# Kernel tuning notes

Measured on AMD Instinct MI355X. Metric: run time of the kernel, lower is better.

The kernel has to match this reference:

```python
import jax, jax.numpy as jnp
import numpy as np

HEADS = 12

def setup_inputs() -> dict:
    key = jax.random.key(0)
    ks = jax.random.split(key, 6)
    dim = 768
    x  = jax.random.normal(ks[0], (2, 4096, dim), dtype=jnp.float32)
    s = dim ** -0.5
    wq = jax.random.normal(ks[1], (dim, dim), dtype=jnp.float32) * s
    wk = jax.random.normal(ks[2], (dim, dim), dtype=jnp.float32) * s
    wv = jax.random.normal(ks[3], (dim, dim), dtype=jnp.float32) * s
    wo = jax.random.normal(ks[4], (dim, dim), dtype=jnp.float32) * s
    bo = jnp.zeros((dim,), dtype=jnp.float32)
    return {"x": x, "wq": wq, "wk": wk, "wv": wv, "wo": wo, "bo": bo}

def reference(x, wq, wk, wv, wo, bo):
    b, n, dim = x.shape
    h = HEADS
    d = dim // h
    scale = d ** -0.5
    # nn.Linear(dim, dim, bias=False): y = x @ W.T ; weights stored [out, in]
    def proj(w):
        return (x @ w.T).reshape(b, n, h, d).transpose(0, 2, 1, 3)  # b h n d
    q, k, v = proj(wq), proj(wk), proj(wv)
    dots = jnp.einsum('bhqd,bhkd->bhqk', q, k) * scale  # full N x N scores
    attn = jax.nn.softmax(dots, axis=-1)
    out = jnp.einsum('bhqk,bhkd->bhqd', attn, v)
    out = out.transpose(0, 2, 1, 3).reshape(b, n, dim)
    # to_out: Linear(dim, dim) + Dropout (identity at inference)
    return out @ wo.T + bo
```

## Files before the change

### kernel.cpp

```cpp
#include <hip/hip_runtime.h>
#include <hip/hip_bf16.h>


#define HEADS 12
#define NSEQ  4096
#define DIM   768
#define DH    64
#define BATCH 2
#define QSCALE 0.18033688f

typedef __attribute__((ext_vector_type(8))) short bf16x8;
typedef __attribute__((ext_vector_type(4))) float f32x4;
typedef __attribute__((ext_vector_type(4))) short bf16x4;

static __device__ __forceinline__ short f2bf(float f) {
    __hip_bfloat16 h = __float2bfloat16(f);
    return *reinterpret_cast<short*>(&h);
}

#define NX (BATCH*NSEQ*DIM)
#define NW (DIM*DIM)

__global__ __launch_bounds__(256) void convert_kernel(
    const float* __restrict__ x,  const float* __restrict__ wq,
    const float* __restrict__ wk, const float* __restrict__ wv,
    const float* __restrict__ wo,
    short* __restrict__ xb, short* __restrict__ wqb, short* __restrict__ wkb,
    short* __restrict__ wvb, short* __restrict__ wob)
{
    int i = (blockIdx.x * 256 + threadIdx.x) * 4;
    const float* src; short* dst; int off;
    if      (i < NX)          { src = x;  dst = xb;  off = i; }
    else if (i < NX + NW)     { src = wq; dst = wqb; off = i - NX; }
    else if (i < NX + 2*NW)   { src = wk; dst = wkb; off = i - NX - NW; }
    else if (i < NX + 3*NW)   { src = wv; dst = wvb; off = i - NX - 2*NW; }
    else                      { src = wo; dst = wob; off = i - NX - 3*NW; }
    float4 f = *(const float4*)(src + off);
    bf16x4 o; o[0] = f2bf(f.x); o[1] = f2bf(f.y); o[2] = f2bf(f.z); o[3] = f2bf(f.w);
    *(bf16x4*)(dst + off) = o;
}

__global__ __launch_bounds__(256, 4) void qkv_proj_kernel(
    const short* __restrict__ xb, const short* __restrict__ wqb,
    const short* __restrict__ wkb, const short* __restrict__ wvb,
    short* __restrict__ qb, short* __restrict__ kb, short* __restrict__ vtb)
{
    __shared__ __align__(16) short As[2][128*32];
    __shared__ __align__(16) short Bs[2][128*32];

    const int wave = threadIdx.x >> 6, lane = threadIdx.x & 63;
    const int lr = lane & 15, lq = lane >> 4;
    const int which = blockIdx.y / 6;
    const short* __restrict__ W = (which == 0) ? wqb : ((which == 1) ? wkb : wvb);
    const int m0  = blockIdx.x * 128;
    const int o0l = (blockIdx.y % 6) * 128;

    const int t  = threadIdx.x;
    const int sr = t >> 2, sc = t & 3;
    const int scs = (sc ^ (sr & 3)) * 8;
    const short* __restrict__ gA = xb + (size_t)(m0  + sr) * DIM + sc*8;
    const short* __restrict__ gB = W  + (size_t)(o0l + sr) * DIM + sc*8;

    const int wm = (wave & 1) * 64, wn = (wave >> 1) * 64;
    const int rsw = (lq ^ (lr & 3)) * 8;

    f32x4 acc[4][4];
    #pragma unroll
    for (int i = 0; i < 4; i++)
        #pragma unroll
        for (int j = 0; j < 4; j++) acc[i][j] = (f32x4){0.f, 0.f, 0.f, 0.f};

    bf16x8 ra0 = *(const bf16x8*)(gA);
    bf16x8 ra1 = *(const bf16x8*)(gA + (size_t)64*DIM);
    bf16x8 rb0 = *(const bf16x8*)(gB);
    bf16x8 rb1 = *(const bf16x8*)(gB + (size_t)64*DIM);
    *(bf16x8*)&As[0][ sr     *32 + scs] = ra0;
    *(bf16x8*)&As[0][(sr+64) *32 + scs] = ra1;
    *(bf16x8*)&Bs[0][ sr     *32 + scs] = rb0;
    *(bf16x8*)&Bs[0][(sr+64) *32 + scs] = rb1;
    __syncthreads();

    for (int kt = 0; kt < 24; kt++) {
        const int p = kt & 1;
        if (kt < 23) {
            const int k1 = (kt + 1) * 32;
            ra0 = *(const bf16x8*)(gA + k1);
            ra1 = *(const bf16x8*)(gA + (size_t)64*DIM + k1);
            rb0 = *(const bf16x8*)(gB + k1);
            rb1 = *(const bf16x8*)(gB + (size_t)64*DIM + k1);
        }
        bf16x8 a[4], b[4];
        #pragma unroll
        for (int i = 0; i < 4; i++)
            a[i] = *(const bf16x8*)&As[p][(wm + i*16 + lr)*32 + rsw];
        #pragma unroll
        for (int j = 0; j < 4; j++)
            b[j] = *(const bf16x8*)&Bs[p][(wn + j*16 + lr)*32 + rsw];
        #pragma unroll
        for (int i = 0; i < 4; i++)
            #pragma unroll
            for (int j = 0; j < 4; j++)
                acc[i][j] = __builtin_amdgcn_mfma_f32_16x16x32_bf16(a[i], b[j], acc[i][j], 0, 0, 0);
        if (kt < 23) {
            *(bf16x8*)&As[1-p][ sr     *32 + scs] = ra0;
            *(bf16x8*)&As[1-p][(sr+64) *32 + scs] = ra1;
            *(bf16x8*)&Bs[1-p][ sr     *32 + scs] = rb0;
            *(bf16x8*)&Bs[1-p][(sr+64) *32 + scs] = rb1;
        }
        __syncthreads();
    }

    if (which == 2) {
        #pragma unroll
        for (int i = 0; i < 4; i++)
            #pragma unroll
            for (int j = 0; j < 4; j++) {
                const int mb = m0 + wm + i*16 + lq*4;
                const int o  = o0l + wn + j*16 + lr;
                const int bb = mb >> 12, n0 = mb & (NSEQ - 1);
                const int h  = o >> 6,   dd = o & 63;
                bf16x4 v;
                #pragma unroll
                for (int r = 0; r < 4; r++) v[r] = f2bf(acc[i][j][r]);
                *(bf16x4*)(vtb + ((size_t)(bb*HEADS + h) * DH + dd) * NSEQ + n0) = v;
            }
    } else {
        short* __restrict__ dst = (which == 0) ? qb : kb;
        const float scale = (which == 0) ? QSCALE : 1.0f;
        #pragma unroll
        for (int i = 0; i < 4; i++)
            #pragma unroll
            for (int j = 0; j < 4; j++)
                #pragma unroll
                for (int r = 0; r < 4; r++) {
                    const int m  = m0 + wm + i*16 + lq*4 + r;
                    const int o  = o0l + wn + j*16 + lr;
                    const int bb = m >> 12, n = m & (NSEQ - 1);
                    const int h  = o >> 6,  dd = o & 63;
                    dst[(((size_t)(bb*HEADS + h) * NSEQ) + n) * DH + dd] = f2bf(acc[i][j][r] * scale);
                }
    }
}

__global__ __launch_bounds__(256, 3) void attn_kernel(
    const short* __restrict__ qb, const short* __restrict__ kb,
    const short* __restrict__ vtb, short* __restrict__ ob)
{
    __shared__ __align__(16) short Ks[2][64*64];
    __shared__ __align__(16) short Vs[2][64*64];
    __shared__ __align__(16) short Vones[16*64];
    __shared__ __align__(16) short Ps[4][2][16*64];

    const int wave = threadIdx.x >> 6, lane = threadIdx.x & 63;
    const int lrow = lane & 15, lquad = lane >> 4;

    const int flat = blockIdx.x;
    const int xcd  = flat & 7;
    const int idx  = flat >> 3;
    const int bh   = xcd * 3 + (idx % 3);
    const int qblk = idx / 3;
    const int b = bh / HEADS, h = bh % HEADS;
    const int q0 = qblk * 128 + wave * 32;

    const short* __restrict__ Q  = qb  + (size_t)bh * NSEQ * DH;
    const short* __restrict__ K  = kb  + (size_t)bh * NSEQ * DH;
    const short* __restrict__ Vt = vtb + (size_t)bh * DH * NSEQ;

    for (int i = threadIdx.x; i < 16*64; i += 256) Vones[i] = 0x3F80;

    const int t  = threadIdx.x;
    const int r2 = t >> 3, cc = t & 7;
    const int ccs = (cc ^ (r2 & 7)) * 8;

    bf16x8 aq[2][2];
    #pragma unroll
    for (int rb = 0; rb < 2; rb++)
        #pragma unroll
        for (int kk = 0; kk < 2; kk++)
            aq[rb][kk] = *(const bf16x8*)(Q + (size_t)(q0 + rb*16 + lrow) * DH + kk*32 + lquad*8);

    f32x4 oacc[2][5];
    #pragma unroll
    for (int rb = 0; rb < 2; rb++)
        #pragma unroll
        for (int ct = 0; ct < 5; ct++) oacc[rb][ct] = (f32x4){0.f, 0.f, 0.f, 0.f};

    {
        bf16x8 k0a = *(const bf16x8*)(K  + (size_t)(r2     ) * DH   + cc*8);
        bf16x8 k0b = *(const bf16x8*)(K  + (size_t)(r2 + 32) * DH   + cc*8);
        bf16x8 v0a = *(const bf16x8*)(Vt + (size_t)(r2     ) * NSEQ + cc*8);
        bf16x8 v0b = *(const bf16x8*)(Vt + (size_t)(r2 + 32) * NSEQ + cc*8);
        *(bf16x8*)&Ks[0][ r2     *64 + ccs] = k0a;
        *(bf16x8*)&Ks[0][(r2+32) *64 + ccs] = k0b;
        *(bf16x8*)&Vs[0][ r2     *64 + ccs] = v0a;
        *(bf16x8*)&Vs[0][(r2+32) *64 + ccs] = v0b;
    }
    __syncthreads();

    for (int kt = 0; kt < NSEQ / 64; kt++) {
        const int p = kt & 1;
        bf16x8 kr0, kr1, vr0, vr1;
        if (kt + 1 < NSEQ / 64) {
            const int key1 = (kt + 1) * 64;
            kr0 = *(const bf16x8*)(K  + (size_t)(key1 + r2     ) * DH   + cc*8);
            kr1 = *(const bf16x8*)(K  + (size_t)(key1 + r2 + 32) * DH   + cc*8);
            vr0 = *(const bf16x8*)(Vt + (size_t)(r2     ) * NSEQ + key1 + cc*8);
            vr1 = *(const bf16x8*)(Vt + (size_t)(r2 + 32) * NSEQ + key1 + cc*8);
        }

        bf16x8 ak[4][2];
        #pragma unroll
        for (int ct = 0; ct < 4; ct++)
            #pragma unroll
            for (int kk = 0; kk < 2; kk++)
                ak[ct][kk] = *(const bf16x8*)&Ks[p][(ct*16 + lrow)*64 + (((kk*4 + lquad) ^ (lrow & 7)) * 8)];

        #pragma unroll
        for (int rb = 0; rb < 2; rb++) {
            f32x4 s[4];
            #pragma unroll
            for (int ct = 0; ct < 4; ct++) s[ct] = (f32x4){0.f, 0.f, 0.f, 0.f};
            #pragma unroll
            for (int kk = 0; kk < 2; kk++)
                #pragma unroll
                for (int ct = 0; ct < 4; ct++)
                    s[ct] = __builtin_amdgcn_mfma_f32_16x16x32_bf16(ak[ct][kk], aq[rb][kk], s[ct], 0, 0, 0);
            #pragma unroll
            for (int ct = 0; ct < 4; ct++) {
                bf16x4 pk;
                #pragma unroll
                for (int r = 0; r < 4; r++) pk[r] = f2bf(exp2f(s[ct][r]));
                const int cps = (((ct*2 + (lquad >> 1)) ^ (lrow & 7)) * 8) + (lquad & 1) * 4;
                *(bf16x4*)&Ps[wave][rb][lrow*64 + cps] = pk;
            }
        }

        bf16x8 bv[5][2];
        #pragma unroll
        for (int ct = 0; ct < 4; ct++)
            #pragma unroll
            for (int kk = 0; kk < 2; kk++)
                bv[ct][kk] = *(const bf16x8*)&Vs[p][(ct*16 + lrow)*64 + (((kk*4 + lquad) ^ (lrow & 7)) * 8)];
        #pragma unroll
        for (int kk = 0; kk < 2; kk++)
            bv[4][kk] = *(const bf16x8*)&Vones[lrow*64 + (((kk*4 + lquad) ^ (lrow & 7)) * 8)];

        #pragma unroll
        for (int rb = 0; rb < 2; rb++) {
            bf16x8 ap[2];
            #pragma unroll
            for (int kk = 0; kk < 2; kk++)
                ap[kk] = *(const bf16x8*)&Ps[wave][rb][lrow*64 + (((kk*4 + lquad) ^ (lrow & 7)) * 8)];
            #pragma unroll
            for (int kk = 0; kk < 2; kk++)
                #pragma unroll
                for (int ct = 0; ct < 5; ct++)
                    oacc[rb][ct] = __builtin_amdgcn_mfma_f32_16x16x32_bf16(ap[kk], bv[ct][kk], oacc[rb][ct], 0, 0, 0);
        }

        if (kt + 1 < NSEQ / 64) {
            *(bf16x8*)&Ks[1-p][ r2     *64 + ccs] = kr0;
            *(bf16x8*)&Ks[1-p][(r2+32) *64 + ccs] = kr1;
            *(bf16x8*)&Vs[1-p][ r2     *64 + ccs] = vr0;
            *(bf16x8*)&Vs[1-p][(r2+32) *64 + ccs] = vr1;
        }
        __syncthreads();
    }

    #pragma unroll
    for (int rb = 0; rb < 2; rb++)
        #pragma unroll
        for (int r = 0; r < 4; r++) {
            const float inv = 1.0f / oacc[rb][4][r];
            const int n = q0 + rb*16 + lquad*4 + r;
            #pragma unroll
            for (int ct = 0; ct < 4; ct++) {
                const int col = h*DH + ct*16 + lrow;
                ob[((size_t)b * NSEQ + n) * DIM + col] = f2bf(oacc[rb][ct][r] * inv);
            }
        }
}

__global__ __launch_bounds__(256, 4) void out_proj_kernel(
    const short* __restrict__ xo, const short* __restrict__ W,
    const float* __restrict__ bias, float* __restrict__ y)
{
    __shared__ __align__(16) short As[2][128*32];
    __shared__ __align__(16) short Bs[2][128*32];

    const int wave = threadIdx.x >> 6, lane = threadIdx.x & 63;
    const int lr = lane & 15, lq = lane >> 4;
    const int m0 = blockIdx.x * 128;
    const int o0 = blockIdx.y * 128;

    const int t  = threadIdx.x;
    const int sr = t >> 2, sc = t & 3;
    const int scs = (sc ^ (sr & 3)) * 8;
    const short* __restrict__ gA = xo + (size_t)(m0 + sr) * DIM + sc*8;
    const short* __restrict__ gB = W  + (size_t)(o0 + sr) * DIM + sc*8;

    const int wm = (wave & 1) * 64, wn = (wave >> 1) * 64;
    const int rsw = (lq ^ (lr & 3)) * 8;

    f32x4 acc[4][4];
    #pragma unroll
    for (int i = 0; i < 4; i++)
        #pragma unroll
        for (int j = 0; j < 4; j++) acc[i][j] = (f32x4){0.f, 0.f, 0.f, 0.f};

    bf16x8 ra0 = *(const bf16x8*)(gA);
    bf16x8 ra1 = *(const bf16x8*)(gA + (size_t)64*DIM);
    bf16x8 rb0 = *(const bf16x8*)(gB);
    bf16x8 rb1 = *(const bf16x8*)(gB + (size_t)64*DIM);
    *(bf16x8*)&As[0][ sr     *32 + scs] = ra0;
    *(bf16x8*)&As[0][(sr+64) *32 + scs] = ra1;
    *(bf16x8*)&Bs[0][ sr     *32 + scs] = rb0;
    *(bf16x8*)&Bs[0][(sr+64) *32 + scs] = rb1;
    __syncthreads();

    for (int kt = 0; kt < 24; kt++) {
        const int p = kt & 1;
        if (kt < 23) {
            const int k1 = (kt + 1) * 32;
            ra0 = *(const bf16x8*)(gA + k1);
            ra1 = *(const bf16x8*)(gA + (size_t)64*DIM + k1);
            rb0 = *(const bf16x8*)(gB + k1);
            rb1 = *(const bf16x8*)(gB + (size_t)64*DIM + k1);
        }
        bf16x8 a[4], b[4];
        #pragma unroll
        for (int i = 0; i < 4; i++)
            a[i] = *(const bf16x8*)&As[p][(wm + i*16 + lr)*32 + rsw];
        #pragma unroll
        for (int j = 0; j < 4; j++)
            b[j] = *(const bf16x8*)&Bs[p][(wn + j*16 + lr)*32 + rsw];
        #pragma unroll
        for (int i = 0; i < 4; i++)
            #pragma unroll
            for (int j = 0; j < 4; j++)
                acc[i][j] = __builtin_amdgcn_mfma_f32_16x16x32_bf16(a[i], b[j], acc[i][j], 0, 0, 0);
        if (kt < 23) {
            *(bf16x8*)&As[1-p][ sr     *32 + scs] = ra0;
            *(bf16x8*)&As[1-p][(sr+64) *32 + scs] = ra1;
            *(bf16x8*)&Bs[1-p][ sr     *32 + scs] = rb0;
            *(bf16x8*)&Bs[1-p][(sr+64) *32 + scs] = rb1;
        }
        __syncthreads();
    }

    #pragma unroll
    for (int i = 0; i < 4; i++)
        #pragma unroll
        for (int j = 0; j < 4; j++)
            #pragma unroll
            for (int r = 0; r < 4; r++) {
                const int m = m0 + wm + i*16 + lq*4 + r;
                const int o = o0 + wn + j*16 + lr;
                y[(size_t)m * DIM + o] = acc[i][j][r] + bias[o];
            }
}

extern "C" void kernel_launch(void* const* d_in, const int* in_sizes, int n_in,
                              void* d_out, int out_size, void* d_ws, size_t ws_size,
                              hipStream_t stream) {
    const float* x  = (const float*)d_in[0];
    const float* wq = (const float*)d_in[1];
    const float* wk = (const float*)d_in[2];
    const float* wv = (const float*)d_in[3];
    const float* wo = (const float*)d_in[4];
    const float* bo = (const float*)d_in[5];
    float* out = (float*)d_out;

    const size_t qkv_elems = (size_t)BATCH * HEADS * NSEQ * DH;
    short* xb  = (short*)d_ws;
    short* wqb = xb  + NX;
    short* wkb = wqb + NW;
    short* wvb = wkb + NW;
    short* wob = wvb + NW;
    short* qb  = wob + NW;
    short* kb  = qb  + qkv_elems;
    short* vtb = kb  + qkv_elems;
    short* ob  = xb;

    dim3 blk(256);
    convert_kernel <<<dim3((NX + 4*NW) / 1024), blk, 0, stream>>>(x, wq, wk, wv, wo,
                                                                  xb, wqb, wkb, wvb, wob);
    qkv_proj_kernel<<<dim3(64, 18), blk, 0, stream>>>(xb, wqb, wkb, wvb, qb, kb, vtb);
    attn_kernel    <<<dim3(768), blk, 0, stream>>>(qb, kb, vtb, ob);
    out_proj_kernel<<<dim3(64, 6), blk, 0, stream>>>(ob, wob, bo, out);
}
```

Measured before the change: 300.9 us.

## Use direct global-to-LDS loads in projections and cheaper exp/pack in attention

Result: faster. 280.9 us (-6.6%).

```diff
diff --git a/kernel.cpp b/kernel.cpp
--- a/kernel.cpp
+++ b/kernel.cpp
@@ -17,6 +17,17 @@
     __hip_bfloat16 h = __float2bfloat16(f);
     return *reinterpret_cast<short*>(&h);
 }
+
+static __device__ __forceinline__ unsigned pkbf(float a, float b) {
+    unsigned ua = __float_as_uint(a), ub = __float_as_uint(b);
+    ua += 0x7FFFu + ((ua >> 16) & 1u);
+    ub += 0x7FFFu + ((ub >> 16) & 1u);
+    return __builtin_amdgcn_perm(ub, ua, 0x07060302);
+}
+
+#define GLL(g, l) __builtin_amdgcn_global_load_lds( \
+    (const __attribute__((address_space(1))) void*)(g), \
+    (__attribute__((address_space(3))) void*)(l), 16, 0, 0)
 
 #define NX (BATCH*NSEQ*DIM)
 #define NW (DIM*DIM)
@@ -55,14 +66,10 @@
     const int m0  = blockIdx.x * 128;
     const int o0l = (blockIdx.y % 6) * 128;
 
-    const int t  = threadIdx.x;
-    const int sr = t >> 2, sc = t & 3;
-    const int scs = (sc ^ (sr & 3)) * 8;
-    const short* __restrict__ gA = xb + (size_t)(m0  + sr) * DIM + sc*8;
-    const short* __restrict__ gB = W  + (size_t)(o0l + sr) * DIM + sc*8;
+    const short* __restrict__ gA = xb + (size_t)(m0  + wave*32 + (lane>>2)) * DIM + (lane&3)*8;
+    const short* __restrict__ gB = W  + (size_t)(o0l + wave*32 + (lane>>2)) * DIM + (lane&3)*8;
 
     const int wm = (wave & 1) * 64, wn = (wave >> 1) * 64;
-    const int rsw = (lq ^ (lr & 3)) * 8;
 
     f32x4 acc[4][4];
     #pragma unroll
@@ -70,43 +77,33 @@
         #pragma unroll
         for (int j = 0; j < 4; j++) acc[i][j] = (f32x4){0.f, 0.f, 0.f, 0.f};
 
-    bf16x8 ra0 = *(const bf16x8*)(gA);
-    bf16x8 ra1 = *(const bf16x8*)(gA + (size_t)64*DIM);
-    bf16x8 rb0 = *(const bf16x8*)(gB);
-    bf16x8 rb1 = *(const bf16x8*)(gB + (size_t)64*DIM);
-    *(bf16x8*)&As[0][ sr     *32 + scs] = ra0;
-    *(bf16x8*)&As[0][(sr+64) *32 + scs] = ra1;
-    *(bf16x8*)&Bs[0][ sr     *32 + scs] = rb0;
-    *(bf16x8*)&Bs[0][(sr+64) *32 + scs] = rb1;
+    GLL(gA,            &As[0][(wave*32     )*32]);
+    GLL(gA + 16*DIM,   &As[0][(wave*32 + 16)*32]);
+    GLL(gB,            &Bs[0][(wave*32     )*32]);
+    GLL(gB + 16*DIM,   &Bs[0][(wave*32 + 16)*32]);
     __syncthreads();
 
     for (int kt = 0; kt < 24; kt++) {
         const int p = kt & 1;
         if (kt < 23) {
             const int k1 = (kt + 1) * 32;
-            ra0 = *(const bf16x8*)(gA + k1);
-            ra1 = *(const bf16x8*)(gA + (size_t)64*DIM + k1);
-            rb0 = *(const bf16x8*)(gB + k1);
-            rb1 = *(const bf16x8*)(gB + (size_t)64*DIM + k1);
+            GLL(gA + k1,          &As[1-p][(wave*32     )*32]);
+            GLL(gA + k1 + 16*DIM, &As[1-p][(wave*32 + 16)*32]);
+            GLL(gB + k1,          &Bs[1-p][(wave*32     )*32]);
+            GLL(gB + k1 + 16*DIM, &Bs[1-p][(wave*32 + 16)*32]);
         }
         bf16x8 a[4], b[4];
         #pragma unroll
         for (int i = 0; i < 4; i++)
-            a[i] = *(const bf16x8*)&As[p][(wm + i*16 + lr)*32 + rsw];
+            a[i] = *(const bf16x8*)&As[p][(wm + i*16 + lr)*32 + lq*8];
         #pragma unroll
         for (int j = 0; j < 4; j++)
-            b[j] = *(const bf16x8*)&Bs[p][(wn + j*16 + lr)*32 + rsw];
+            b[j] = *(const bf16x8*)&Bs[p][(wn + j*16 + lr)*32 + lq*8];
         #pragma unroll
         for (int i = 0; i < 4; i++)
             #pragma unroll
             for (int j = 0; j < 4; j++)
                 acc[i][j] = __builtin_amdgcn_mfma_f32_16x16x32_bf16(a[i], b[j], acc[i][j], 0, 0, 0);
-        if (kt < 23) {
-            *(bf16x8*)&As[1-p][ sr     *32 + scs] = ra0;
-            *(bf16x8*)&As[1-p][(sr+64) *32 + scs] = ra1;
-            *(bf16x8*)&Bs[1-p][ sr     *32 + scs] = rb0;
-            *(bf16x8*)&Bs[1-p][(sr+64) *32 + scs] = rb1;
-        }
         __syncthreads();
     }
 
@@ -197,6 +194,11 @@
     }
     __syncthreads();
 
+    bf16x8 bv4[2];
+    #pragma unroll
+    for (int kk = 0; kk < 2; kk++)
+        bv4[kk] = *(const bf16x8*)&Vones[lrow*64 + (((kk*4 + lquad) ^ (lrow & 7)) * 8)];
+
     for (int kt = 0; kt < NSEQ / 64; kt++) {
         const int p = kt & 1;
         bf16x8 kr0, kr1, vr0, vr1;
@@ -227,23 +229,22 @@
                     s[ct] = __builtin_amdgcn_mfma_f32_16x16x32_bf16(ak[ct][kk], aq[rb][kk], s[ct], 0, 0, 0);
             #pragma unroll
             for (int ct = 0; ct < 4; ct++) {
-                bf16x4 pk;
-                #pragma unroll
-                for (int r = 0; r < 4; r++) pk[r] = f2bf(exp2f(s[ct][r]));
+                const float e0 = __builtin_amdgcn_exp2f(s[ct][0]);
+                const float e1 = __builtin_amdgcn_exp2f(s[ct][1]);
+                const float e2 = __builtin_amdgcn_exp2f(s[ct][2]);
+                const float e3 = __builtin_amdgcn_exp2f(s[ct][3]);
+                const unsigned lo = pkbf(e0, e1), hi = pkbf(e2, e3);
                 const int cps = (((ct*2 + (lquad >> 1)) ^ (lrow & 7)) * 8) + (lquad & 1) * 4;
-                *(bf16x4*)&Ps[wave][rb][lrow*64 + cps] = pk;
-            }
-        }
-
-        bf16x8 bv[5][2];
+                *(uint2*)&Ps[wave][rb][lrow*64 + cps] = (uint2){lo, hi};
+            }
+        }
+
+        bf16x8 bv[4][2];
         #pragma unroll
         for (int ct = 0; ct < 4; ct++)
             #pragma unroll
             for (int kk = 0; kk < 2; kk++)
                 bv[ct][kk] = *(const bf16x8*)&Vs[p][(ct*16 + lrow)*64 + (((kk*4 + lquad) ^ (lrow & 7)) * 8)];
-        #pragma unroll
-        for (int kk = 0; kk < 2; kk++)
-            bv[4][kk] = *(const bf16x8*)&Vones[lrow*64 + (((kk*4 + lquad) ^ (lrow & 7)) * 8)];
 
         #pragma unroll
         for (int rb = 0; rb < 2; rb++) {
@@ -252,10 +253,12 @@
             for (int kk = 0; kk < 2; kk++)
                 ap[kk] = *(const bf16x8*)&Ps[wave][rb][lrow*64 + (((kk*4 + lquad) ^ (lrow & 7)) * 8)];
             #pragma unroll
-            for (int kk = 0; kk < 2; kk++)
+            for (int kk = 0; kk < 2; kk++) {
                 #pragma unroll
-                for (int ct = 0; ct < 5; ct++)
+                for (int ct = 0; ct < 4; ct++)
                     oacc[rb][ct] = __builtin_amdgcn_mfma_f32_16x16x32_bf16(ap[kk], bv[ct][kk], oacc[rb][ct], 0, 0, 0);
+                oacc[rb][4] = __builtin_amdgcn_mfma_f32_16x16x32_bf16(ap[kk], bv4[kk], oacc[rb][4], 0, 0, 0);
+            }
         }
 
         if (kt + 1 < NSEQ / 64) {
@@ -271,7 +274,7 @@
     for (int rb = 0; rb < 2; rb++)
         #pragma unroll
         for (int r = 0; r < 4; r++) {
-            const float inv = 1.0f / oacc[rb][4][r];
+            const float inv = __builtin_amdgcn_rcpf(oacc[rb][4][r]);
             const int n = q0 + rb*16 + lquad*4 + r;
             #pragma unroll
             for (int ct = 0; ct < 4; ct++) {
@@ -293,14 +296,10 @@
     const int m0 = blockIdx.x * 128;
     const int o0 = blockIdx.y * 128;
 
-    const int t  = threadIdx.x;
-    const int sr = t >> 2, sc = t & 3;
-    const int scs = (sc ^ (sr & 3)) * 8;
-    const short* __restrict__ gA = xo + (size_t)(m0 + sr) * DIM + sc*8;
-    const short* __restrict__ gB = W  + (size_t)(o0 + sr) * DIM + sc*8;
+    const short* __restrict__ gA = xo + (size_t)(m0 + wave*32 + (lane>>2)) * DIM + (lane&3)*8;
+    const short* __restrict__ gB = W  + (size_t)(o0 + wave*32 + (lane>>2)) * DIM + (lane&3)*8;
 
     const int wm = (wave & 1) * 64, wn = (wave >> 1) * 64;
-    const int rsw = (lq ^ (lr & 3)) * 8;
 
     f32x4 acc[4][4];
     #pragma unroll
@@ -308,43 +307,33 @@
         #pragma unroll
         for (int j = 0; j < 4; j++) acc[i][j] = (f32x4){0.f, 0.f, 0.f, 0.f};
 
-    bf16x8 ra0 = *(const bf16x8*)(gA);
-    bf16x8 ra1 = *(const bf16x8*)(gA + (size_t)64*DIM);
-    bf16x8 rb0 = *(const bf16x8*)(gB);
-    bf16x8 rb1 = *(const bf16x8*)(gB + (size_t)64*DIM);
-    *(bf16x8*)&As[0][ sr     *32 + scs] = ra0;
-    *(bf16x8*)&As[0][(sr+64) *32 + scs] = ra1;
-    *(bf16x8*)&Bs[0][ sr     *32 + scs] = rb0;
-    *(bf16x8*)&Bs[0][(sr+64) *32 + scs] = rb1;
+    GLL(gA,            &As[0][(wave*32     )*32]);
+    GLL(gA + 16*DIM,   &As[0][(wave*32 + 16)*32]);
+    GLL(gB,            &Bs[0][(wave*32     )*32]);
+    GLL(gB + 16*DIM,   &Bs[0][(wave*32 + 16)*32]);
     __syncthreads();
 
     for (int kt = 0; kt < 24; kt++) {
         const int p = kt & 1;
         if (kt < 23) {
             const int k1 = (kt + 1) * 32;
-            ra0 = *(const bf16x8*)(gA + k1);
-            ra1 = *(const bf16x8*)(gA + (size_t)64*DIM + k1);
-            rb0 = *(const bf16x8*)(gB + k1);
-            rb1 = *(const bf16x8*)(gB + (size_t)64*DIM + k1);
+            GLL(gA + k1,          &As[1-p][(wave*32     )*32]);
+            GLL(gA + k1 + 16*DIM, &As[1-p][(wave*32 + 16)*32]);
+            GLL(gB + k1,          &Bs[1-p][(wave*32     )*32]);
+            GLL(gB + k1 + 16*DIM, &Bs[1-p][(wave*32 + 16)*32]);
         }
         bf16x8 a[4], b[4];
         #pragma unroll
         for (int i = 0; i < 4; i++)
-            a[i] = *(const bf16x8*)&As[p][(wm + i*16 + lr)*32 + rsw];
+            a[i] = *(const bf16x8*)&As[p][(wm + i*16 + lr)*32 + lq*8];
         #pragma unroll
         for (int j = 0; j < 4; j++)
-            b[j] = *(const bf16x8*)&Bs[p][(wn + j*16 + lr)*32 + rsw];
+            b[j] = *(const bf16x8*)&Bs[p][(wn + j*16 + lr)*32 + lq*8];
         #pragma unroll
         for (int i = 0; i < 4; i++)
             #pragma unroll
             for (int j = 0; j < 4; j++)
                 acc[i][j] = __builtin_amdgcn_mfma_f32_16x16x32_bf16(a[i], b[j], acc[i][j], 0, 0, 0);
-        if (kt < 23) {
-            *(bf16x8*)&As[1-p][ sr     *32 + scs] = ra0;
-            *(bf16x8*)&As[1-p][(sr+64) *32 + scs] = ra1;
-            *(bf16x8*)&Bs[1-p][ sr     *32 + scs] = rb0;
-            *(bf16x8*)&Bs[1-p][(sr+64) *32 + scs] = rb1;
-        }
         __syncthreads();
     }
 
```
